# Kernel optimization log

Measured on AMD Instinct MI355X. Metric: run time of the kernel, lower is better.

Reference implementation:

```python
import jax, jax.numpy as jnp
import numpy as np

HEADS = 4
DIM_HEAD = 64
QUERY_DIM = 512
CONTEXT_DIM = 512
INNER = HEADS * DIM_HEAD  # 256
SCALE = DIM_HEAD ** -0.5


def setup_inputs() -> dict:
    key = jax.random.key(0)
    ks = jax.random.split(key, 9)
    b, n, m = 4, 2048, 2048
    inp = {
        'x1': jax.random.normal(ks[0], (b, n, QUERY_DIM), jnp.float32),
        'x2': jax.random.normal(ks[1], (b, n, QUERY_DIM), jnp.float32),
        'context': jax.random.normal(ks[2], (b, m, CONTEXT_DIM), jnp.float32),
        # weights stored [in, out] (= torch weight.T)
        'Wq': jax.random.normal(ks[3], (QUERY_DIM, INNER), jnp.float32) * (QUERY_DIM ** -0.5),
        'Wq2': jax.random.normal(ks[4], (QUERY_DIM, INNER), jnp.float32) * (QUERY_DIM ** -0.5),
        'Wk': jax.random.normal(ks[5], (CONTEXT_DIM, INNER), jnp.float32) * (CONTEXT_DIM ** -0.5),
        'Wv': jax.random.normal(ks[6], (CONTEXT_DIM, INNER), jnp.float32) * (CONTEXT_DIM ** -0.5),
        'Wo': jax.random.normal(ks[7], (INNER, QUERY_DIM), jnp.float32) * (INNER ** -0.5),
        'bo': jax.random.normal(ks[8], (QUERY_DIM,), jnp.float32) * 0.01,
    }
    return inp


def _split_heads(t):
    # [b, n, h*d] -> [b, h, n, d]
    b, n, _ = t.shape
    return t.reshape(b, n, HEADS, DIM_HEAD).transpose(0, 2, 1, 3)


def reference(x1, x2, context, Wq, Wq2, Wk, Wv, Wo, bo):
    q = _split_heads(x1 @ Wq)
    q2 = _split_heads(x2 @ Wq2)
    k = _split_heads(context @ Wk)
    v = _split_heads(context @ Wv)
    sim = jnp.einsum('bhid,bhjd->bhij', q, k) * SCALE
    sim2 = jnp.einsum('bhid,bhjd->bhij', q2, k) * SCALE
    attn = 0.3 * jax.nn.softmax(sim, axis=-1) + 0.7 * jax.nn.softmax(sim2, axis=-1)
    out = jnp.einsum('bhij,bhjd->bhid', attn, v)  # [b, h, n, d]
    b, h, n, d = out.shape
    out = out.transpose(0, 2, 1, 3).reshape(b, n, h * d)
    return out @ Wo + bo
```

## Files before the change

kernel.cpp:

```cpp
#include <hip/hip_runtime.h>

typedef __attribute__((ext_vector_type(8))) short bf16x8;
typedef __attribute__((ext_vector_type(4))) float f32x4;
typedef unsigned short ushort_t;
typedef unsigned int uint_t;

__device__ __forceinline__ ushort_t f2bf(float f) {
    unsigned int x = __builtin_bit_cast(unsigned int, f);
    x += 0x7fffu + ((x >> 16) & 1u);
    return (ushort_t)(x >> 16);
}
__device__ __forceinline__ uint_t pack2(float a, float b) {
    return (uint_t)f2bf(a) | ((uint_t)f2bf(b) << 16);
}

#define LOG2E 1.4426950408889634f

#define WT_OFF   0
#define WOT_OFF  524288
#define QKV_OFF  655360
#define QKV_SZ   2097152
#define QKV_OFF_Z3 (3 * (size_t)QKV_SZ)
#define O_OFF    9043968

__global__ __launch_bounds__(256) void transpose_w(
    const float* __restrict__ Wq, const float* __restrict__ Wq2,
    const float* __restrict__ Wk, const float* __restrict__ Wv,
    const float* __restrict__ Wo, ushort_t* __restrict__ ws)
{
    const int j = blockIdx.y;
    const int t = blockIdx.x * 256 + threadIdx.x;
    const float* in;
    ushort_t* out;
    int C;
    if (j < 4) {
        in = (j == 0) ? Wq : (j == 1) ? Wq2 : (j == 2) ? Wk : Wv;
        out = ws + WT_OFF + (size_t)j * 131072;
        C = 256;
    } else {
        in = Wo; out = ws + WOT_OFF; C = 512;
    }
    const int R = 131072 / C;
    const int r = t / C, c = t % C;
    out[(size_t)c * R + r] = f2bf(in[t]);
}

__global__ __launch_bounds__(256) void proj_gemm(
    const float* __restrict__ x1, const float* __restrict__ x2,
    const float* __restrict__ ctx, const ushort_t* __restrict__ Wt,
    ushort_t* __restrict__ QKV)
{
    __shared__ __align__(16) ushort_t lA[64 * 40];
    __shared__ __align__(16) ushort_t lB[256 * 40];
    const int z = blockIdx.y;
    const float* A = (z == 0) ? x1 : (z == 1) ? x2 : ctx;
    const ushort_t* Bt = Wt + (size_t)z * 131072;
    const float sc = (z < 2) ? (0.125f * LOG2E) : 1.0f;
    const int tid = threadIdx.x;
    const int wave = tid >> 6, lane = tid & 63;
    const int quad = lane >> 4, l16 = lane & 15;
    const size_t row0 = (size_t)blockIdx.x * 64;
    const int sr = tid >> 2, sc8 = (tid & 3) << 3;

    f32x4 acc[16] = {};
    for (int k0 = 0; k0 < 512; k0 += 32) {
        const float* src = A + (row0 + sr) * 512 + k0 + sc8;
        float4 v0 = *(const float4*)src;
        float4 v1 = *(const float4*)(src + 4);
        ushort_t tmp[8] = { f2bf(v0.x), f2bf(v0.y), f2bf(v0.z), f2bf(v0.w),
                            f2bf(v1.x), f2bf(v1.y), f2bf(v1.z), f2bf(v1.w) };
        *(uint4*)&lA[sr * 40 + sc8] = *(const uint4*)tmp;
#pragma unroll
        for (int rr = 0; rr < 4; ++rr)
            *(uint4*)&lB[(rr * 64 + sr) * 40 + sc8] =
                *(const uint4*)(Bt + (size_t)(rr * 64 + sr) * 512 + k0 + sc8);
        __syncthreads();
        bf16x8 af = *(const bf16x8*)&lA[(wave * 16 + l16) * 40 + quad * 8];
#pragma unroll
        for (int c = 0; c < 16; ++c) {
            bf16x8 bfr = *(const bf16x8*)&lB[(c * 16 + l16) * 40 + quad * 8];
            acc[c] = __builtin_amdgcn_mfma_f32_16x16x32_bf16(af, bfr, acc[c], 0, 0, 0);
        }
        __syncthreads();
    }
    if (z == 3) {
        const int b = (int)(row0 >> 11);
        const int tokl = ((int)row0 & 2047) + wave * 16 + quad * 4;
        ushort_t* Vt = QKV + QKV_OFF_Z3;
#pragma unroll
        for (int c = 0; c < 16; ++c) {
            const int col = c * 16 + l16;
            const int h = col >> 6, d = col & 63;
            uint2 w;
            w.x = pack2(acc[c][0], acc[c][1]);
            w.y = pack2(acc[c][2], acc[c][3]);
            *(uint2*)(Vt + ((size_t)((b * 4 + h) * 64 + d)) * 2048 + tokl) = w;
        }
    } else {
        ushort_t* C = QKV + (size_t)z * QKV_SZ;
#pragma unroll
        for (int c = 0; c < 16; ++c) {
            const int col = c * 16 + l16;
#pragma unroll
            for (int r = 0; r < 4; ++r)
                C[(row0 + wave * 16 + quad * 4 + r) * 256 + col] = f2bf(acc[c][r] * sc);
        }
    }
}

__global__ __launch_bounds__(256) void out_gemm(
    const ushort_t* __restrict__ Op, const ushort_t* __restrict__ Wot,
    const float* __restrict__ bias, float* __restrict__ out)
{
    __shared__ __align__(16) ushort_t lA[64 * 40];
    __shared__ __align__(16) ushort_t lB[256 * 40];
    const int tid = threadIdx.x;
    const int wave = tid >> 6, lane = tid & 63;
    const int quad = lane >> 4, l16 = lane & 15;
    const size_t row0 = (size_t)blockIdx.x * 64;
    const int col0 = blockIdx.y * 256;
    const int sr = tid >> 2, sc8 = (tid & 3) << 3;

    f32x4 acc[16] = {};
    for (int k0 = 0; k0 < 256; k0 += 32) {
        *(uint4*)&lA[sr * 40 + sc8] = *(const uint4*)(Op + (row0 + sr) * 256 + k0 + sc8);
#pragma unroll
        for (int rr = 0; rr < 4; ++rr)
            *(uint4*)&lB[(rr * 64 + sr) * 40 + sc8] =
                *(const uint4*)(Wot + (size_t)(col0 + rr * 64 + sr) * 256 + k0 + sc8);
        __syncthreads();
        bf16x8 af = *(const bf16x8*)&lA[(wave * 16 + l16) * 40 + quad * 8];
#pragma unroll
        for (int c = 0; c < 16; ++c) {
            bf16x8 bfr = *(const bf16x8*)&lB[(c * 16 + l16) * 40 + quad * 8];
            acc[c] = __builtin_amdgcn_mfma_f32_16x16x32_bf16(af, bfr, acc[c], 0, 0, 0);
        }
        __syncthreads();
    }
#pragma unroll
    for (int c = 0; c < 16; ++c) {
        const int col = col0 + c * 16 + l16;
        const float bv = bias[col];
#pragma unroll
        for (int r = 0; r < 4; ++r)
            out[(row0 + wave * 16 + quad * 4 + r) * 512 + col] = acc[c][r] + bv;
    }
}


#define ATTN_STAGE(MB, BUF) do {                                                        \
    _Pragma("unroll")                                                                   \
    for (int it_ = 0; it_ < 2; ++it_) {                                                 \
        const int cc_ = tid + it_ * 256;                                                \
        const int g_ = (cc_ ^ (cc_ >> 3)) & 7;                                          \
        const ushort_t* kp_ = Kb + (size_t)(tok0 + (MB) + (cc_ >> 3)) * 256 + in0 + g_ * 8; \
        __builtin_amdgcn_global_load_lds(                                               \
            (const __attribute__((address_space(1))) void*)kp_,                         \
            (__attribute__((address_space(3))) void*)&lK[BUF][cc_ * 8], 16, 0, 0);      \
        const ushort_t* vp_ = Vt + (size_t)(bh64 + (cc_ >> 3)) * 2048 + (MB) + g_ * 8;  \
        __builtin_amdgcn_global_load_lds(                                               \
            (const __attribute__((address_space(1))) void*)vp_,                         \
            (__attribute__((address_space(3))) void*)&lV[BUF][cc_ * 8], 16, 0, 0);      \
    }                                                                                   \
} while (0)

#define ATTN_ITER(I, P) do {                                                            \
    __syncthreads();                                                                    \
    { const int mn_ = ((I) + 1) * 64; if (mn_ < 2048) ATTN_STAGE(mn_, 1 - (P)); }       \
    f32x4 st1[4] = {}, st2[4] = {};                                                     \
    _Pragma("unroll")                                                                   \
    for (int c = 0; c < 4; ++c) {                                                       \
        _Pragma("unroll")                                                               \
        for (int ks = 0; ks < 2; ++ks) {                                                \
            bf16x8 kf = *(const bf16x8*)&lK[P][(c * 16 + l16) * 64 +                    \
                                              ((((ks * 4 + quad) ^ l7) & 7) << 3)];     \
            st1[c] = __builtin_amdgcn_mfma_f32_16x16x32_bf16(kf, q1f[ks], st1[c], 0, 0, 0); \
            st2[c] = __builtin_amdgcn_mfma_f32_16x16x32_bf16(kf, q2f[ks], st2[c], 0, 0, 0); \
        } }                                                                             \
    _Pragma("unroll")                                                                   \
    for (int c = 0; c < 4; ++c) {                                                       \
        float p0 = __builtin_amdgcn_exp2f(st1[c][0]);                                   \
        float p1 = __builtin_amdgcn_exp2f(st1[c][1]);                                   \
        float p2 = __builtin_amdgcn_exp2f(st1[c][2]);                                   \
        float p3 = __builtin_amdgcn_exp2f(st1[c][3]);                                   \
        l1 += (p0 + p1) + (p2 + p3);                                                    \
        uint2 w; w.x = pack2(p0, p1); w.y = pack2(p2, p3);                              \
        *(uint2*)&lPw0[l16 * 72 + c * 16 + quad * 4] = w;                               \
        float r0 = __builtin_amdgcn_exp2f(st2[c][0]);                                   \
        float r1 = __builtin_amdgcn_exp2f(st2[c][1]);                                   \
        float r2 = __builtin_amdgcn_exp2f(st2[c][2]);                                   \
        float r3 = __builtin_amdgcn_exp2f(st2[c][3]);                                   \
        l2 += (r0 + r1) + (r2 + r3);                                                    \
        uint2 y; y.x = pack2(r0, r1); y.y = pack2(r2, r3);                              \
        *(uint2*)&lPw1[l16 * 72 + c * 16 + quad * 4] = y;                               \
    }                                                                                   \
    bf16x8 pa1[2], pa2[2];                                                              \
    _Pragma("unroll")                                                                   \
    for (int ks = 0; ks < 2; ++ks) {                                                    \
        pa1[ks] = *(const bf16x8*)&lPw0[l16 * 72 + ks * 32 + quad * 8];                 \
        pa2[ks] = *(const bf16x8*)&lPw1[l16 * 72 + ks * 32 + quad * 8];                 \
    }                                                                                   \
    _Pragma("unroll")                                                                   \
    for (int c = 0; c < 4; ++c) {                                                       \
        _Pragma("unroll")                                                               \
        for (int ks = 0; ks < 2; ++ks) {                                                \
            bf16x8 vf = *(const bf16x8*)&lV[P][(c * 16 + l16) * 64 +                    \
                                              ((((ks * 4 + quad) ^ l7) & 7) << 3)];     \
            o1[c] = __builtin_amdgcn_mfma_f32_16x16x32_bf16(vf, pa1[ks], o1[c], 0, 0, 0); \
            o2[c] = __builtin_amdgcn_mfma_f32_16x16x32_bf16(vf, pa2[ks], o2[c], 0, 0, 0); \
        } }                                                                             \
} while (0)

__global__ __launch_bounds__(256) void attn_fused(
    const ushort_t* __restrict__ Qb, const ushort_t* __restrict__ Q2b,
    const ushort_t* __restrict__ Kb, const ushort_t* __restrict__ Vt,
    ushort_t* __restrict__ Ob)
{
    __shared__ __align__(16) ushort_t lK[2][64 * 64];
    __shared__ __align__(16) ushort_t lV[2][64 * 64];
    __shared__ __align__(16) ushort_t lP[4][2][16 * 72];

    const int qt = blockIdx.x;
    const int bh = blockIdx.y;
    const int tid = threadIdx.x;
    const int wave = tid >> 6, lane = tid & 63;
    const int quad = lane >> 4, l16 = lane & 15;
    const int l7 = l16 & 7;
    const size_t tok0 = (size_t)(bh >> 2) * 2048;
    const int in0 = (bh & 3) * 64;
    const int bh64 = bh * 64;
    ushort_t* lPw0 = &lP[wave][0][0];
    ushort_t* lPw1 = &lP[wave][1][0];

    bf16x8 q1f[2], q2f[2];
    {
        const ushort_t* qr1 = Qb  + (tok0 + qt * 64 + wave * 16 + l16) * 256 + in0;
        const ushort_t* qr2 = Q2b + (tok0 + qt * 64 + wave * 16 + l16) * 256 + in0;
#pragma unroll
        for (int ks = 0; ks < 2; ++ks) {
            q1f[ks] = *(const bf16x8*)(qr1 + ks * 32 + quad * 8);
            q2f[ks] = *(const bf16x8*)(qr2 + ks * 32 + quad * 8);
        }
    }

    ATTN_STAGE(0, 0);

    f32x4 o1[4] = {}, o2[4] = {};
    float l1 = 0.f, l2 = 0.f;

    for (int i = 0; i < 32; i += 2) {
        ATTN_ITER(i, 0);
        ATTN_ITER(i + 1, 1);
    }

    l1 += __shfl_xor(l1, 16, 64); l1 += __shfl_xor(l1, 32, 64);
    l2 += __shfl_xor(l2, 16, 64); l2 += __shfl_xor(l2, 32, 64);
    const float inv1 = 0.3f / l1, inv2 = 0.7f / l2;

    ushort_t* orow = Ob + (tok0 + qt * 64 + wave * 16 + l16) * 256 + in0;
#pragma unroll
    for (int c = 0; c < 4; ++c) {
        const float f0 = o1[c][0] * inv1 + o2[c][0] * inv2;
        const float f1 = o1[c][1] * inv1 + o2[c][1] * inv2;
        const float f2 = o1[c][2] * inv1 + o2[c][2] * inv2;
        const float f3 = o1[c][3] * inv1 + o2[c][3] * inv2;
        uint2 w; w.x = pack2(f0, f1); w.y = pack2(f2, f3);
        *(uint2*)(orow + c * 16 + quad * 4) = w;
    }
}

extern "C" void kernel_launch(void* const* d_in, const int* in_sizes, int n_in,
                              void* d_out, int out_size, void* d_ws, size_t ws_size,
                              hipStream_t stream)
{
    (void)in_sizes; (void)n_in; (void)out_size; (void)ws_size;
    const float* x1  = (const float*)d_in[0];
    const float* x2  = (const float*)d_in[1];
    const float* ctx = (const float*)d_in[2];
    const float* Wq  = (const float*)d_in[3];
    const float* Wq2 = (const float*)d_in[4];
    const float* Wk  = (const float*)d_in[5];
    const float* Wv  = (const float*)d_in[6];
    const float* Wo  = (const float*)d_in[7];
    const float* bo  = (const float*)d_in[8];
    ushort_t* ws  = (ushort_t*)d_ws;
    float* out = (float*)d_out;

    ushort_t* Wt  = ws + WT_OFF;
    ushort_t* Wot = ws + WOT_OFF;
    ushort_t* QKV = ws + QKV_OFF;
    ushort_t* Q   = QKV;
    ushort_t* Q2  = QKV + 1 * (size_t)QKV_SZ;
    ushort_t* Kp  = QKV + 2 * (size_t)QKV_SZ;
    ushort_t* Vt  = QKV + 3 * (size_t)QKV_SZ;
    ushort_t* Op  = ws + O_OFF;

    transpose_w<<<dim3(512, 5), 256, 0, stream>>>(Wq, Wq2, Wk, Wv, Wo, ws);
    proj_gemm  <<<dim3(128, 4), 256, 0, stream>>>(x1, x2, ctx, Wt, QKV);
    attn_fused <<<dim3(32, 16), 256, 0, stream>>>(Q, Q2, Kp, Vt, Op);
    out_gemm   <<<dim3(128, 2), 256, 0, stream>>>(Op, Wot, bo, out);
}
```

Baseline: 195.6 us.

## Fuse all stages into one persistent kernel with grid barriers

Merges the weight transpose, QKV projection, attention and output GEMM into a single 512-block persistent kernel separated by atomic-counter grid barriers, removing three kernel launch gaps. Projection and output GEMMs now stage weights with direct global-to-LDS loads, double-buffering and swizzled layouts, and prefetch A in registers. Attention gains a triple-buffered K/V pipeline that overlaps the PV product of the previous tile with the QK product of the current one, plus a reordered block-to-head mapping. The bf16 conversion uses the hardware cast. Grid barriers depend on all 512 blocks being co-resident (two per CU) and add a memset launch.

New measurement: 595.0 us. +204.2%, slower.

```diff
diff --git a/kernel.cpp b/kernel.cpp
--- a/kernel.cpp
+++ b/kernel.cpp
@@ -6,9 +6,7 @@
 typedef unsigned int uint_t;
 
 __device__ __forceinline__ ushort_t f2bf(float f) {
-    unsigned int x = __builtin_bit_cast(unsigned int, f);
-    x += 0x7fffu + ((x >> 16) & 1u);
-    return (ushort_t)(x >> 16);
+    return __builtin_bit_cast(ushort_t, (__bf16)f);
 }
 __device__ __forceinline__ uint_t pack2(float a, float b) {
     return (uint_t)f2bf(a) | ((uint_t)f2bf(b) << 16);
@@ -22,27 +20,285 @@
 #define QKV_SZ   2097152
 #define QKV_OFF_Z3 (3 * (size_t)QKV_SZ)
 #define O_OFF    9043968
+#define CTR_USHORT 11141120
+#define CTR_BYTES  (22282240ull)
+#define WS_NEEDED  (CTR_BYTES + 192)
+
+#define PROJ_STAGE_P(K0, LBP) do {                                                   \
+    _Pragma("unroll")                                                                \
+    for (int it_ = 0; it_ < 8; ++it_) {                                              \
+        const int cc_ = tid + it_ * 256;                                             \
+        const int g_ = (cc_ ^ (cc_ >> 3)) & 7;                                       \
+        const ushort_t* bp_ = Bt + (size_t)(cc_ >> 3) * 512 + (K0) + g_ * 8;         \
+        __builtin_amdgcn_global_load_lds(                                            \
+            (const __attribute__((address_space(1))) void*)bp_,                      \
+            (__attribute__((address_space(3))) void*)&(LBP)[cc_ * 8], 16, 0, 0);     \
+    }                                                                                \
+} while (0)
+
+#define OUT_STAGE_P(K0, LBP) do {                                                    \
+    _Pragma("unroll")                                                                \
+    for (int it_ = 0; it_ < 4; ++it_) {                                              \
+        const int cc_ = tid + it_ * 256;                                             \
+        const int g_ = (cc_ ^ (cc_ >> 3)) & 7;                                       \
+        const ushort_t* bp_ = Wot + (size_t)(col0 + (cc_ >> 3)) * 256 + (K0) + g_ * 8; \
+        __builtin_amdgcn_global_load_lds(                                            \
+            (const __attribute__((address_space(1))) void*)bp_,                      \
+            (__attribute__((address_space(3))) void*)&(LBP)[cc_ * 8], 16, 0, 0);     \
+    }                                                                                \
+} while (0)
+
+#define ATTN_STAGE(MB, KDST, VDST) do {                                                 \
+    _Pragma("unroll")                                                                   \
+    for (int it_ = 0; it_ < 2; ++it_) {                                                 \
+        const int cc_ = tid + it_ * 256;                                                \
+        const int g_ = (cc_ ^ (cc_ >> 3)) & 7;                                          \
+        const ushort_t* kp_ = Kb + (size_t)(tok0 + (MB) + (cc_ >> 3)) * 256 + in0 + g_ * 8; \
+        __builtin_amdgcn_global_load_lds(                                               \
+            (const __attribute__((address_space(1))) void*)kp_,                         \
+            (__attribute__((address_space(3))) void*)&(KDST)[cc_ * 8], 16, 0, 0);       \
+        const ushort_t* vp_ = Vt + (size_t)(bh64 + (cc_ >> 3)) * 2048 + (MB) + g_ * 8;  \
+        __builtin_amdgcn_global_load_lds(                                               \
+            (const __attribute__((address_space(1))) void*)vp_,                         \
+            (__attribute__((address_space(3))) void*)&(VDST)[cc_ * 8], 16, 0, 0);       \
+    }                                                                                   \
+} while (0)
+
+#define ATTN_BODY(LKB, LVB, LPB)                                                        \
+    ushort_t* lPw0 = (LPB) + wave * 2304;                                               \
+    ushort_t* lPw1 = lPw0 + 1152;                                                       \
+    bf16x8 q1f[2], q2f[2];                                                              \
+    {                                                                                   \
+        const ushort_t* qr1 = Qb  + (tok0 + qt * 64 + wave * 16 + l16) * 256 + in0;     \
+        const ushort_t* qr2 = Q2b + (tok0 + qt * 64 + wave * 16 + l16) * 256 + in0;     \
+        _Pragma("unroll")                                                               \
+        for (int ks = 0; ks < 2; ++ks) {                                                \
+            q1f[ks] = *(const bf16x8*)(qr1 + ks * 32 + quad * 8);                       \
+            q2f[ks] = *(const bf16x8*)(qr2 + ks * 32 + quad * 8);                       \
+        }                                                                               \
+    }                                                                                   \
+    ushort_t* pKcur = (LKB);        ushort_t* pVcur = (LVB);                            \
+    ushort_t* pKpre = (LKB) + 4096; ushort_t* pVpre = (LVB) + 4096;                     \
+    ushort_t* pKold = (LKB) + 8192; ushort_t* pVold = (LVB) + 8192;                     \
+    ATTN_STAGE(0, pKcur, pVcur);                                                        \
+    f32x4 o1[4] = {}, o2[4] = {};                                                       \
+    bf16x8 pa1[2], pa2[2];                                                              \
+    float l1 = 0.f, l2 = 0.f;                                                           \
+    for (int i = 0; i < 32; ++i) {                                                      \
+        __syncthreads();                                                                \
+        if (i < 31) ATTN_STAGE((i + 1) * 64, pKpre, pVpre);                             \
+        f32x4 st1[4] = {}, st2[4] = {};                                                 \
+        _Pragma("unroll")                                                               \
+        for (int c = 0; c < 4; ++c) {                                                   \
+            _Pragma("unroll")                                                           \
+            for (int ks = 0; ks < 2; ++ks) {                                            \
+                bf16x8 kf = *(const bf16x8*)&pKcur[(c * 16 + l16) * 64 +                \
+                                                   ((((ks * 4 + quad) ^ l7) & 7) << 3)];\
+                st1[c] = __builtin_amdgcn_mfma_f32_16x16x32_bf16(kf, q1f[ks], st1[c], 0, 0, 0); \
+                st2[c] = __builtin_amdgcn_mfma_f32_16x16x32_bf16(kf, q2f[ks], st2[c], 0, 0, 0); \
+            }                                                                           \
+        }                                                                               \
+        if (i > 0) {                                                                    \
+            _Pragma("unroll")                                                           \
+            for (int c = 0; c < 4; ++c) {                                               \
+                _Pragma("unroll")                                                       \
+                for (int ks = 0; ks < 2; ++ks) {                                        \
+                    bf16x8 vf = *(const bf16x8*)&pVold[(c * 16 + l16) * 64 +            \
+                                                       ((((ks * 4 + quad) ^ l7) & 7) << 3)]; \
+                    o1[c] = __builtin_amdgcn_mfma_f32_16x16x32_bf16(vf, pa1[ks], o1[c], 0, 0, 0); \
+                    o2[c] = __builtin_amdgcn_mfma_f32_16x16x32_bf16(vf, pa2[ks], o2[c], 0, 0, 0); \
+                }                                                                       \
+            }                                                                           \
+        }                                                                               \
+        _Pragma("unroll")                                                               \
+        for (int c = 0; c < 4; ++c) {                                                   \
+            float p0 = __builtin_amdgcn_exp2f(st1[c][0]);                               \
+            float p1 = __builtin_amdgcn_exp2f(st1[c][1]);                               \
+            float p2 = __builtin_amdgcn_exp2f(st1[c][2]);                               \
+            float p3 = __builtin_amdgcn_exp2f(st1[c][3]);                               \
+            l1 += (p0 + p1) + (p2 + p3);                                                \
+            uint2 w2; w2.x = pack2(p0, p1); w2.y = pack2(p2, p3);                       \
+            *(uint2*)&lPw0[l16 * 72 + c * 16 + quad * 4] = w2;                          \
+            float r0 = __builtin_amdgcn_exp2f(st2[c][0]);                               \
+            float r1 = __builtin_amdgcn_exp2f(st2[c][1]);                               \
+            float r2 = __builtin_amdgcn_exp2f(st2[c][2]);                               \
+            float r3 = __builtin_amdgcn_exp2f(st2[c][3]);                               \
+            l2 += (r0 + r1) + (r2 + r3);                                                \
+            uint2 y; y.x = pack2(r0, r1); y.y = pack2(r2, r3);                          \
+            *(uint2*)&lPw1[l16 * 72 + c * 16 + quad * 4] = y;                           \
+        }                                                                               \
+        _Pragma("unroll")                                                               \
+        for (int ks = 0; ks < 2; ++ks) {                                                \
+            pa1[ks] = *(const bf16x8*)&lPw0[l16 * 72 + ks * 32 + quad * 8];             \
+            pa2[ks] = *(const bf16x8*)&lPw1[l16 * 72 + ks * 32 + quad * 8];             \
+        }                                                                               \
+        ushort_t* tK = pKold; pKold = pKcur; pKcur = pKpre; pKpre = tK;                 \
+        ushort_t* tV = pVold; pVold = pVcur; pVcur = pVpre; pVpre = tV;                 \
+    }                                                                                   \
+    _Pragma("unroll")                                                                   \
+    for (int c = 0; c < 4; ++c) {                                                       \
+        _Pragma("unroll")                                                               \
+        for (int ks = 0; ks < 2; ++ks) {                                                \
+            bf16x8 vf = *(const bf16x8*)&pVold[(c * 16 + l16) * 64 +                    \
+                                               ((((ks * 4 + quad) ^ l7) & 7) << 3)];    \
+            o1[c] = __builtin_amdgcn_mfma_f32_16x16x32_bf16(vf, pa1[ks], o1[c], 0, 0, 0); \
+            o2[c] = __builtin_amdgcn_mfma_f32_16x16x32_bf16(vf, pa2[ks], o2[c], 0, 0, 0); \
+        }                                                                               \
+    }                                                                                   \
+    l1 += __shfl_xor(l1, 16, 64); l1 += __shfl_xor(l1, 32, 64);                         \
+    l2 += __shfl_xor(l2, 16, 64); l2 += __shfl_xor(l2, 32, 64);                         \
+    const float inv1 = 0.3f / l1, inv2 = 0.7f / l2;                                     \
+    ushort_t* orow = Ob + (tok0 + qt * 64 + wave * 16 + l16) * 256 + in0;               \
+    _Pragma("unroll")                                                                   \
+    for (int c = 0; c < 4; ++c) {                                                       \
+        const float f0 = o1[c][0] * inv1 + o2[c][0] * inv2;                             \
+        const float f1 = o1[c][1] * inv1 + o2[c][1] * inv2;                             \
+        const float f2 = o1[c][2] * inv1 + o2[c][2] * inv2;                             \
+        const float f3 = o1[c][3] * inv1 + o2[c][3] * inv2;                             \
+        uint2 w2; w2.x = pack2(f0, f1); w2.y = pack2(f2, f3);                           \
+        *(uint2*)(orow + c * 16 + quad * 4) = w2;                                       \
+    }
+
+#define PROJ_BODY(LB0, LB1)                                                             \
+    PROJ_STAGE_P(0, (LB0));                                                             \
+    const float* arow = A + (row0 + wave * 16 + l16) * 512 + quad * 8;                  \
+    float4 a[4];                                                                        \
+    a[0] = *(const float4*)(arow);                                                      \
+    a[1] = *(const float4*)(arow + 4);                                                  \
+    a[2] = *(const float4*)(arow + 32);                                                 \
+    a[3] = *(const float4*)(arow + 36);                                                 \
+    f32x4 acc[16] = {};                                                                 \
+    for (int k0 = 0; k0 < 512; k0 += 64) {                                              \
+        const int pb = (k0 >> 6) & 1;                                                   \
+        ushort_t* lbp = pb ? (LB1) : (LB0);                                             \
+        __syncthreads();                                                                \
+        if (k0 + 64 < 512) { ushort_t* lbn = pb ? (LB0) : (LB1); PROJ_STAGE_P(k0 + 64, lbn); } \
+        float4 n[4] = {a[0], a[1], a[2], a[3]};                                         \
+        if (k0 + 64 < 512) {                                                            \
+            n[0] = *(const float4*)(arow + k0 + 64);                                    \
+            n[1] = *(const float4*)(arow + k0 + 68);                                    \
+            n[2] = *(const float4*)(arow + k0 + 96);                                    \
+            n[3] = *(const float4*)(arow + k0 + 100);                                   \
+        }                                                                               \
+        bf16x8 af[2];                                                                   \
+        _Pragma("unroll")                                                               \
+        for (int ks = 0; ks < 2; ++ks) {                                                \
+            uint4 aw;                                                                   \
+            aw.x = pack2(a[2 * ks].x, a[2 * ks].y);                                     \
+            aw.y = pack2(a[2 * ks].z, a[2 * ks].w);                                     \
+            aw.z = pack2(a[2 * ks + 1].x, a[2 * ks + 1].y);                             \
+            aw.w = pack2(a[2 * ks + 1].z, a[2 * ks + 1].w);                             \
+            af[ks] = __builtin_bit_cast(bf16x8, aw);                                    \
+        }                                                                               \
+        _Pragma("unroll")                                                               \
+        for (int c = 0; c < 16; ++c) {                                                  \
+            _Pragma("unroll")                                                           \
+            for (int ks = 0; ks < 2; ++ks) {                                            \
+                bf16x8 bfr = *(const bf16x8*)&lbp[(c * 16 + l16) * 64 +                 \
+                                                  (((ks * 4 + quad) ^ l7) << 3)];       \
+                acc[c] = __builtin_amdgcn_mfma_f32_16x16x32_bf16(af[ks], bfr, acc[c], 0, 0, 0); \
+            }                                                                           \
+        }                                                                               \
+        a[0] = n[0]; a[1] = n[1]; a[2] = n[2]; a[3] = n[3];                             \
+    }                                                                                   \
+    if (z == 3) {                                                                       \
+        const int b = (int)(row0 >> 11);                                                \
+        const int tokl = ((int)row0 & 2047) + wave * 16 + quad * 4;                     \
+        ushort_t* Vtw = QKV + QKV_OFF_Z3;                                               \
+        _Pragma("unroll")                                                               \
+        for (int c = 0; c < 16; ++c) {                                                  \
+            const int col = c * 16 + l16;                                               \
+            const int h = col >> 6, d = col & 63;                                       \
+            uint2 w2;                                                                   \
+            w2.x = pack2(acc[c][0], acc[c][1]);                                         \
+            w2.y = pack2(acc[c][2], acc[c][3]);                                         \
+            *(uint2*)(Vtw + ((size_t)((b * 4 + h) * 64 + d)) * 2048 + tokl) = w2;       \
+        }                                                                               \
+    } else {                                                                            \
+        ushort_t* C = QKV + (size_t)z * QKV_SZ;                                         \
+        _Pragma("unroll")                                                               \
+        for (int c = 0; c < 16; ++c) {                                                  \
+            const int col = c * 16 + l16;                                               \
+            _Pragma("unroll")                                                           \
+            for (int r = 0; r < 4; ++r)                                                 \
+                C[(row0 + wave * 16 + quad * 4 + r) * 256 + col] = f2bf(acc[c][r] * sc);\
+        }                                                                               \
+    }
+
+#define OUT_BODY(LB0, LB1)                                                              \
+    OUT_STAGE_P(0, (LB0));                                                              \
+    const ushort_t* arow = Op + (row0 + wave * 16 + l16) * 256 + quad * 8;              \
+    bf16x8 af0 = *(const bf16x8*)(arow);                                                \
+    bf16x8 af1 = *(const bf16x8*)(arow + 32);                                           \
+    f32x4 acc[8] = {};                                                                  \
+    for (int k0 = 0; k0 < 256; k0 += 64) {                                              \
+        const int pb = (k0 >> 6) & 1;                                                   \
+        ushort_t* lbp = pb ? (LB1) : (LB0);                                             \
+        __syncthreads();                                                                \
+        if (k0 + 64 < 256) { ushort_t* lbn = pb ? (LB0) : (LB1); OUT_STAGE_P(k0 + 64, lbn); } \
+        bf16x8 an0 = af0, an1 = af1;                                                    \
+        if (k0 + 64 < 256) {                                                            \
+            an0 = *(const bf16x8*)(arow + k0 + 64);                                     \
+            an1 = *(const bf16x8*)(arow + k0 + 96);                                     \
+        }                                                                               \
+        _Pragma("unroll")                                                               \
+        for (int c = 0; c < 8; ++c) {                                                   \
+            bf16x8 b0 = *(const bf16x8*)&lbp[(c * 16 + l16) * 64 + ((quad ^ l7) << 3)]; \
+            acc[c] = __builtin_amdgcn_mfma_f32_16x16x32_bf16(af0, b0, acc[c], 0, 0, 0); \
+            bf16x8 b1 = *(const bf16x8*)&lbp[(c * 16 + l16) * 64 + (((4 + quad) ^ l7) << 3)]; \
+            acc[c] = __builtin_amdgcn_mfma_f32_16x16x32_bf16(af1, b1, acc[c], 0, 0, 0); \
+        }                                                                               \
+        af0 = an0; af1 = an1;                                                           \
+    }                                                                                   \
+    _Pragma("unroll")                                                                   \
+    for (int c = 0; c < 8; ++c) {                                                       \
+        const int col = col0 + c * 16 + l16;                                            \
+        const float bv = bias[col];                                                     \
+        _Pragma("unroll")                                                               \
+        for (int r = 0; r < 4; ++r)                                                     \
+            out[(row0 + wave * 16 + quad * 4 + r) * 512 + col] = acc[c][r] + bv;        \
+    }
+
+#define TRANS_BODY(LT)                                                                  \
+    const float* in;                                                                    \
+    ushort_t* outp;                                                                     \
+    int C;                                                                              \
+    if (j < 4) {                                                                        \
+        in = (j == 0) ? Wq : (j == 1) ? Wq2 : (j == 2) ? Wk : Wv;                       \
+        outp = ws + WT_OFF + (size_t)j * 131072; C = 256;                               \
+    } else {                                                                            \
+        in = Wo; outp = ws + WOT_OFF; C = 512;                                          \
+    }                                                                                   \
+    const int R = 131072 / C;                                                           \
+    const int tc = C >> 6;                                                              \
+    const int r0 = (bx / tc) * 64, c0 = (bx % tc) * 64;                                 \
+    const int ir = tid >> 4, ic = (tid & 15) * 4;                                       \
+    _Pragma("unroll")                                                                   \
+    for (int i = 0; i < 4; ++i) {                                                       \
+        const int r = ir + i * 16;                                                      \
+        float4 v = *(const float4*)(in + (size_t)(r0 + r) * C + c0 + ic);               \
+        uint2 w2; w2.x = pack2(v.x, v.y); w2.y = pack2(v.z, v.w);                       \
+        *(uint2*)&(LT)[r * 72 + ic] = w2;                                               \
+    }                                                                                   \
+    __syncthreads();                                                                    \
+    const int oc = tid >> 2, rr0 = (tid & 3) * 16;                                      \
+    ushort_t g[16];                                                                     \
+    _Pragma("unroll")                                                                   \
+    for (int k = 0; k < 16; ++k) g[k] = (LT)[(rr0 + k) * 72 + oc];                      \
+    ushort_t* op = outp + (size_t)(c0 + oc) * R + r0 + rr0;                             \
+    *(uint4*)op = *(const uint4*)&g[0];                                                 \
+    *(uint4*)(op + 8) = *(const uint4*)&g[8];
 
 __global__ __launch_bounds__(256) void transpose_w(
     const float* __restrict__ Wq, const float* __restrict__ Wq2,
     const float* __restrict__ Wk, const float* __restrict__ Wv,
     const float* __restrict__ Wo, ushort_t* __restrict__ ws)
 {
+    __shared__ __align__(16) ushort_t lT[64 * 72];
     const int j = blockIdx.y;
-    const int t = blockIdx.x * 256 + threadIdx.x;
-    const float* in;
-    ushort_t* out;
-    int C;
-    if (j < 4) {
-        in = (j == 0) ? Wq : (j == 1) ? Wq2 : (j == 2) ? Wk : Wv;
-        out = ws + WT_OFF + (size_t)j * 131072;
-        C = 256;
-    } else {
-        in = Wo; out = ws + WOT_OFF; C = 512;
-    }
-    const int R = 131072 / C;
-    const int r = t / C, c = t % C;
-    out[(size_t)c * R + r] = f2bf(in[t]);
+    const int bx = blockIdx.x;
+    const int tid = threadIdx.x;
+    TRANS_BODY(lT)
 }
 
 __global__ __launch_bounds__(256) void proj_gemm(
@@ -50,8 +306,7 @@
     const float* __restrict__ ctx, const ushort_t* __restrict__ Wt,
     ushort_t* __restrict__ QKV)
 {
-    __shared__ __align__(16) ushort_t lA[64 * 40];
-    __shared__ __align__(16) ushort_t lB[256 * 40];
+    __shared__ __align__(16) ushort_t lB[2][256 * 64];
     const int z = blockIdx.y;
     const float* A = (z == 0) ? x1 : (z == 1) ? x2 : ctx;
     const ushort_t* Bt = Wt + (size_t)z * 131072;
@@ -59,169 +314,37 @@
     const int tid = threadIdx.x;
     const int wave = tid >> 6, lane = tid & 63;
     const int quad = lane >> 4, l16 = lane & 15;
+    const int l7 = l16 & 7;
     const size_t row0 = (size_t)blockIdx.x * 64;
-    const int sr = tid >> 2, sc8 = (tid & 3) << 3;
-
-    f32x4 acc[16] = {};
-    for (int k0 = 0; k0 < 512; k0 += 32) {
-        const float* src = A + (row0 + sr) * 512 + k0 + sc8;
-        float4 v0 = *(const float4*)src;
-        float4 v1 = *(const float4*)(src + 4);
-        ushort_t tmp[8] = { f2bf(v0.x), f2bf(v0.y), f2bf(v0.z), f2bf(v0.w),
-                            f2bf(v1.x), f2bf(v1.y), f2bf(v1.z), f2bf(v1.w) };
-        *(uint4*)&lA[sr * 40 + sc8] = *(const uint4*)tmp;
-#pragma unroll
-        for (int rr = 0; rr < 4; ++rr)
-            *(uint4*)&lB[(rr * 64 + sr) * 40 + sc8] =
-                *(const uint4*)(Bt + (size_t)(rr * 64 + sr) * 512 + k0 + sc8);
-        __syncthreads();
-        bf16x8 af = *(const bf16x8*)&lA[(wave * 16 + l16) * 40 + quad * 8];
-#pragma unroll
-        for (int c = 0; c < 16; ++c) {
-            bf16x8 bfr = *(const bf16x8*)&lB[(c * 16 + l16) * 40 + quad * 8];
-            acc[c] = __builtin_amdgcn_mfma_f32_16x16x32_bf16(af, bfr, acc[c], 0, 0, 0);
-        }
-        __syncthreads();
-    }
-    if (z == 3) {
-        const int b = (int)(row0 >> 11);
-        const int tokl = ((int)row0 & 2047) + wave * 16 + quad * 4;
-        ushort_t* Vt = QKV + QKV_OFF_Z3;
-#pragma unroll
-        for (int c = 0; c < 16; ++c) {
-            const int col = c * 16 + l16;
-            const int h = col >> 6, d = col & 63;
-            uint2 w;
-            w.x = pack2(acc[c][0], acc[c][1]);
-            w.y = pack2(acc[c][2], acc[c][3]);
-            *(uint2*)(Vt + ((size_t)((b * 4 + h) * 64 + d)) * 2048 + tokl) = w;
-        }
-    } else {
-        ushort_t* C = QKV + (size_t)z * QKV_SZ;
-#pragma unroll
-        for (int c = 0; c < 16; ++c) {
-            const int col = c * 16 + l16;
-#pragma unroll
-            for (int r = 0; r < 4; ++r)
-                C[(row0 + wave * 16 + quad * 4 + r) * 256 + col] = f2bf(acc[c][r] * sc);
-        }
-    }
+    PROJ_BODY(&lB[0][0], &lB[1][0])
 }
 
 __global__ __launch_bounds__(256) void out_gemm(
     const ushort_t* __restrict__ Op, const ushort_t* __restrict__ Wot,
     const float* __restrict__ bias, float* __restrict__ out)
 {
-    __shared__ __align__(16) ushort_t lA[64 * 40];
-    __shared__ __align__(16) ushort_t lB[256 * 40];
+    __shared__ __align__(16) ushort_t lB[2][128 * 64];
     const int tid = threadIdx.x;
     const int wave = tid >> 6, lane = tid & 63;
     const int quad = lane >> 4, l16 = lane & 15;
+    const int l7 = l16 & 7;
     const size_t row0 = (size_t)blockIdx.x * 64;
-    const int col0 = blockIdx.y * 256;
-    const int sr = tid >> 2, sc8 = (tid & 3) << 3;
-
-    f32x4 acc[16] = {};
-    for (int k0 = 0; k0 < 256; k0 += 32) {
-        *(uint4*)&lA[sr * 40 + sc8] = *(const uint4*)(Op + (row0 + sr) * 256 + k0 + sc8);
-#pragma unroll
-        for (int rr = 0; rr < 4; ++rr)
-            *(uint4*)&lB[(rr * 64 + sr) * 40 + sc8] =
-                *(const uint4*)(Wot + (size_t)(col0 + rr * 64 + sr) * 256 + k0 + sc8);
-        __syncthreads();
-        bf16x8 af = *(const bf16x8*)&lA[(wave * 16 + l16) * 40 + quad * 8];
-#pragma unroll
-        for (int c = 0; c < 16; ++c) {
-            bf16x8 bfr = *(const bf16x8*)&lB[(c * 16 + l16) * 40 + quad * 8];
-            acc[c] = __builtin_amdgcn_mfma_f32_16x16x32_bf16(af, bfr, acc[c], 0, 0, 0);
-        }
-        __syncthreads();
-    }
-#pragma unroll
-    for (int c = 0; c < 16; ++c) {
-        const int col = col0 + c * 16 + l16;
-        const float bv = bias[col];
-#pragma unroll
-        for (int r = 0; r < 4; ++r)
-            out[(row0 + wave * 16 + quad * 4 + r) * 512 + col] = acc[c][r] + bv;
-    }
-}
-
-
-#define ATTN_STAGE(MB, BUF) do {                                                        \
-    _Pragma("unroll")                                                                   \
-    for (int it_ = 0; it_ < 2; ++it_) {                                                 \
-        const int cc_ = tid + it_ * 256;                                                \
-        const int g_ = (cc_ ^ (cc_ >> 3)) & 7;                                          \
-        const ushort_t* kp_ = Kb + (size_t)(tok0 + (MB) + (cc_ >> 3)) * 256 + in0 + g_ * 8; \
-        __builtin_amdgcn_global_load_lds(                                               \
-            (const __attribute__((address_space(1))) void*)kp_,                         \
-            (__attribute__((address_space(3))) void*)&lK[BUF][cc_ * 8], 16, 0, 0);      \
-        const ushort_t* vp_ = Vt + (size_t)(bh64 + (cc_ >> 3)) * 2048 + (MB) + g_ * 8;  \
-        __builtin_amdgcn_global_load_lds(                                               \
-            (const __attribute__((address_space(1))) void*)vp_,                         \
-            (__attribute__((address_space(3))) void*)&lV[BUF][cc_ * 8], 16, 0, 0);      \
-    }                                                                                   \
-} while (0)
-
-#define ATTN_ITER(I, P) do {                                                            \
-    __syncthreads();                                                                    \
-    { const int mn_ = ((I) + 1) * 64; if (mn_ < 2048) ATTN_STAGE(mn_, 1 - (P)); }       \
-    f32x4 st1[4] = {}, st2[4] = {};                                                     \
-    _Pragma("unroll")                                                                   \
-    for (int c = 0; c < 4; ++c) {                                                       \
-        _Pragma("unroll")                                                               \
-        for (int ks = 0; ks < 2; ++ks) {                                                \
-            bf16x8 kf = *(const bf16x8*)&lK[P][(c * 16 + l16) * 64 +                    \
-                                              ((((ks * 4 + quad) ^ l7) & 7) << 3)];     \
-            st1[c] = __builtin_amdgcn_mfma_f32_16x16x32_bf16(kf, q1f[ks], st1[c], 0, 0, 0); \
-            st2[c] = __builtin_amdgcn_mfma_f32_16x16x32_bf16(kf, q2f[ks], st2[c], 0, 0, 0); \
-        } }                                                                             \
-    _Pragma("unroll")                                                                   \
-    for (int c = 0; c < 4; ++c) {                                                       \
-        float p0 = __builtin_amdgcn_exp2f(st1[c][0]);                                   \
-        float p1 = __builtin_amdgcn_exp2f(st1[c][1]);                                   \
-        float p2 = __builtin_amdgcn_exp2f(st1[c][2]);                                   \
-        float p3 = __builtin_amdgcn_exp2f(st1[c][3]);                                   \
-        l1 += (p0 + p1) + (p2 + p3);                                                    \
-        uint2 w; w.x = pack2(p0, p1); w.y = pack2(p2, p3);                              \
-        *(uint2*)&lPw0[l16 * 72 + c * 16 + quad * 4] = w;                               \
-        float r0 = __builtin_amdgcn_exp2f(st2[c][0]);                                   \
-        float r1 = __builtin_amdgcn_exp2f(st2[c][1]);                                   \
-        float r2 = __builtin_amdgcn_exp2f(st2[c][2]);                                   \
-        float r3 = __builtin_amdgcn_exp2f(st2[c][3]);                                   \
-        l2 += (r0 + r1) + (r2 + r3);                                                    \
-        uint2 y; y.x = pack2(r0, r1); y.y = pack2(r2, r3);                              \
-        *(uint2*)&lPw1[l16 * 72 + c * 16 + quad * 4] = y;                               \
-    }                                                                                   \
-    bf16x8 pa1[2], pa2[2];                                                              \
-    _Pragma("unroll")                                                                   \
-    for (int ks = 0; ks < 2; ++ks) {                                                    \
-        pa1[ks] = *(const bf16x8*)&lPw0[l16 * 72 + ks * 32 + quad * 8];                 \
-        pa2[ks] = *(const bf16x8*)&lPw1[l16 * 72 + ks * 32 + quad * 8];                 \
-    }                                                                                   \
-    _Pragma("unroll")                                                                   \
-    for (int c = 0; c < 4; ++c) {                                                       \
-        _Pragma("unroll")                                                               \
-        for (int ks = 0; ks < 2; ++ks) {                                                \
-            bf16x8 vf = *(const bf16x8*)&lV[P][(c * 16 + l16) * 64 +                    \
-                                              ((((ks * 4 + quad) ^ l7) & 7) << 3)];     \
-            o1[c] = __builtin_amdgcn_mfma_f32_16x16x32_bf16(vf, pa1[ks], o1[c], 0, 0, 0); \
-            o2[c] = __builtin_amdgcn_mfma_f32_16x16x32_bf16(vf, pa2[ks], o2[c], 0, 0, 0); \
-        } }                                                                             \
-} while (0)
+    const int col0 = blockIdx.y * 128;
+    OUT_BODY(&lB[0][0], &lB[1][0])
+}
 
 __global__ __launch_bounds__(256) void attn_fused(
     const ushort_t* __restrict__ Qb, const ushort_t* __restrict__ Q2b,
     const ushort_t* __restrict__ Kb, const ushort_t* __restrict__ Vt,
     ushort_t* __restrict__ Ob)
 {
-    __shared__ __align__(16) ushort_t lK[2][64 * 64];
-    __shared__ __align__(16) ushort_t lV[2][64 * 64];
+    __shared__ __align__(16) ushort_t lK[3][64 * 64];
+    __shared__ __align__(16) ushort_t lV[3][64 * 64];
     __shared__ __align__(16) ushort_t lP[4][2][16 * 72];
-
-    const int qt = blockIdx.x;
-    const int bh = blockIdx.y;
+    const int bid = blockIdx.x;
+    const int w = bid >> 3;
+    const int qt = w & 31;
+    const int bh = (bid & 7) * 2 + (w >> 5);
     const int tid = threadIdx.x;
     const int wave = tid >> 6, lane = tid & 63;
     const int quad = lane >> 4, l16 = lane & 15;
@@ -229,43 +352,82 @@
     const size_t tok0 = (size_t)(bh >> 2) * 2048;
     const int in0 = (bh & 3) * 64;
     const int bh64 = bh * 64;
-    ushort_t* lPw0 = &lP[wave][0][0];
-    ushort_t* lPw1 = &lP[wave][1][0];
-
-    bf16x8 q1f[2], q2f[2];
+    ATTN_BODY(&lK[0][0], &lV[0][0], &lP[0][0][0])
+}
+
+__device__ __forceinline__ void gridbar(int* ctr, int nblk) {
+    __threadfence();
+    __syncthreads();
+    if (threadIdx.x == 0) {
+        __hip_atomic_fetch_add(ctr, 1, __ATOMIC_RELEASE, __HIP_MEMORY_SCOPE_AGENT);
+        while (__hip_atomic_load(ctr, __ATOMIC_ACQUIRE, __HIP_MEMORY_SCOPE_AGENT) < nblk)
+            __builtin_amdgcn_s_sleep(2);
+    }
+    __syncthreads();
+    __threadfence();
+}
+
+__global__ __launch_bounds__(256, 2) void fused_all(
+    const float* __restrict__ x1, const float* __restrict__ x2,
+    const float* __restrict__ ctx,
+    const float* __restrict__ Wq, const float* __restrict__ Wq2,
+    const float* __restrict__ Wk, const float* __restrict__ Wv,
+    const float* __restrict__ Wo, const float* __restrict__ bo,
+    ushort_t* __restrict__ ws, float* __restrict__ out)
+{
+    __shared__ __align__(16) ushort_t smem[33792];
+
+    const int bid = blockIdx.x;
+    const int tid = threadIdx.x;
+    const int wave = tid >> 6, lane = tid & 63;
+    const int quad = lane >> 4, l16 = lane & 15;
+    const int l7 = l16 & 7;
+
+    int* ctrs = (int*)(ws + CTR_USHORT);
+
+    ushort_t* Wt  = ws + WT_OFF;
+    ushort_t* Wot = ws + WOT_OFF;
+    ushort_t* QKV = ws + QKV_OFF;
+    const ushort_t* Qb  = QKV;
+    const ushort_t* Q2b = QKV + 1 * (size_t)QKV_SZ;
+    const ushort_t* Kb  = QKV + 2 * (size_t)QKV_SZ;
+    const ushort_t* Vt  = QKV + 3 * (size_t)QKV_SZ;
+    ushort_t* Op  = ws + O_OFF;
+
+    if (bid < 160) {
+        const int j = bid >> 5;
+        const int bx = bid & 31;
+        TRANS_BODY(smem)
+    }
+    gridbar(&ctrs[0], 512);
+
     {
-        const ushort_t* qr1 = Qb  + (tok0 + qt * 64 + wave * 16 + l16) * 256 + in0;
-        const ushort_t* qr2 = Q2b + (tok0 + qt * 64 + wave * 16 + l16) * 256 + in0;
-#pragma unroll
-        for (int ks = 0; ks < 2; ++ks) {
-            q1f[ks] = *(const bf16x8*)(qr1 + ks * 32 + quad * 8);
-            q2f[ks] = *(const bf16x8*)(qr2 + ks * 32 + quad * 8);
-        }
-    }
-
-    ATTN_STAGE(0, 0);
-
-    f32x4 o1[4] = {}, o2[4] = {};
-    float l1 = 0.f, l2 = 0.f;
-
-    for (int i = 0; i < 32; i += 2) {
-        ATTN_ITER(i, 0);
-        ATTN_ITER(i + 1, 1);
-    }
-
-    l1 += __shfl_xor(l1, 16, 64); l1 += __shfl_xor(l1, 32, 64);
-    l2 += __shfl_xor(l2, 16, 64); l2 += __shfl_xor(l2, 32, 64);
-    const float inv1 = 0.3f / l1, inv2 = 0.7f / l2;
-
-    ushort_t* orow = Ob + (tok0 + qt * 64 + wave * 16 + l16) * 256 + in0;
-#pragma unroll
-    for (int c = 0; c < 4; ++c) {
-        const float f0 = o1[c][0] * inv1 + o2[c][0] * inv2;
-        const float f1 = o1[c][1] * inv1 + o2[c][1] * inv2;
-        const float f2 = o1[c][2] * inv1 + o2[c][2] * inv2;
-        const float f3 = o1[c][3] * inv1 + o2[c][3] * inv2;
-        uint2 w; w.x = pack2(f0, f1); w.y = pack2(f2, f3);
-        *(uint2*)(orow + c * 16 + quad * 4) = w;
+        const int z = bid >> 7;
+        const float* A = (z == 0) ? x1 : (z == 1) ? x2 : ctx;
+        const ushort_t* Bt = Wt + (size_t)z * 131072;
+        const float sc = (z < 2) ? (0.125f * LOG2E) : 1.0f;
+        const size_t row0 = (size_t)(bid & 127) * 64;
+        PROJ_BODY(smem, smem + 16384)
+    }
+    gridbar(&ctrs[16], 512);
+
+    {
+        const int w = bid >> 3;
+        const int qt = w & 31;
+        const int bh = (bid & 7) * 2 + (w >> 5);
+        const size_t tok0 = (size_t)(bh >> 2) * 2048;
+        const int in0 = (bh & 3) * 64;
+        const int bh64 = bh * 64;
+        ushort_t* Ob = Op;
+        ATTN_BODY(smem, smem + 12288, smem + 24576)
+    }
+    gridbar(&ctrs[32], 512);
+
+    {
+        const float* bias = bo;
+        const size_t row0 = (size_t)(bid & 127) * 64;
+        const int col0 = (bid >> 7) * 128;
+        OUT_BODY(smem, smem + 8192)
     }
 }
 
@@ -273,7 +435,7 @@
                               void* d_out, int out_size, void* d_ws, size_t ws_size,
                               hipStream_t stream)
 {
-    (void)in_sizes; (void)n_in; (void)out_size; (void)ws_size;
+    (void)in_sizes; (void)n_in; (void)out_size;
     const float* x1  = (const float*)d_in[0];
     const float* x2  = (const float*)d_in[1];
     const float* ctx = (const float*)d_in[2];
@@ -286,6 +448,13 @@
     ushort_t* ws  = (ushort_t*)d_ws;
     float* out = (float*)d_out;
 
+    if (ws_size >= WS_NEEDED) {
+        hipMemsetAsync((char*)d_ws + CTR_BYTES, 0, 192, stream);
+        fused_all<<<dim3(512), 256, 0, stream>>>(x1, x2, ctx, Wq, Wq2, Wk, Wv, Wo, bo,
+                                                 ws, out);
+        return;
+    }
+
     ushort_t* Wt  = ws + WT_OFF;
     ushort_t* Wot = ws + WOT_OFF;
     ushort_t* QKV = ws + QKV_OFF;
@@ -295,8 +464,8 @@
     ushort_t* Vt  = QKV + 3 * (size_t)QKV_SZ;
     ushort_t* Op  = ws + O_OFF;
 
-    transpose_w<<<dim3(512, 5), 256, 0, stream>>>(Wq, Wq2, Wk, Wv, Wo, ws);
+    transpose_w<<<dim3(32, 5),  256, 0, stream>>>(Wq, Wq2, Wk, Wv, Wo, ws);
     proj_gemm  <<<dim3(128, 4), 256, 0, stream>>>(x1, x2, ctx, Wt, QKV);
-    attn_fused <<<dim3(32, 16), 256, 0, stream>>>(Q, Q2, Kp, Vt, Op);
-    out_gemm   <<<dim3(128, 2), 256, 0, stream>>>(Op, Wot, bo, out);
-}
+    attn_fused <<<dim3(512),    256, 0, stream>>>(Q, Q2, Kp, Vt, Op);
+    out_gemm   <<<dim3(128, 4), 256, 0, stream>>>(Op, Wot, bo, out);
+}
```
